# Optimization experiments

Measured on AMD Instinct MI355X. Metric: run time of the kernel, lower is better.

Reference implementation:

```python
import jax, jax.numpy as jnp
import numpy as np

HEADS = 16
KV_HEADS = 4
DIM_HEAD = 64
DIM = 1024
B, N = 2, 2048


def setup_inputs() -> dict:
    key = jax.random.key(0)
    k1, k2, k3 = jax.random.split(key, 3)
    x = jax.random.normal(k1, (B, N, DIM), dtype=jnp.float32)
    Wq = jax.random.normal(k2, (DIM, HEADS * DIM_HEAD), dtype=jnp.float32) / np.sqrt(DIM)
    Wkv = jax.random.normal(k3, (DIM, 2 * KV_HEADS * DIM_HEAD), dtype=jnp.float32) / np.sqrt(DIM)
    k_scale = jnp.ones((HEADS, 1, DIM_HEAD), dtype=jnp.float32)
    return {"x": x, "Wq": Wq, "Wkv": Wkv, "k_scale": k_scale}


def reference(x, Wq, Wkv, k_scale):
    b, n, _ = x.shape
    g = HEADS // KV_HEADS  # query heads per kv head
    scale = DIM_HEAD ** -0.5
    # fused qkv projections (no bias)
    q = (x @ Wq).reshape(b, n, HEADS, DIM_HEAD)
    kv = x @ Wkv
    k, v = jnp.split(kv, 2, axis=-1)
    k = k.reshape(b, n, KV_HEADS, DIM_HEAD).transpose(0, 2, 1, 3)  # b k n d
    v = v.reshape(b, n, KV_HEADS, DIM_HEAD).transpose(0, 2, 1, 3)  # b k n d
    # group query heads: b, kv_heads, g, n, d
    qg = q.transpose(0, 2, 1, 3).reshape(b, KV_HEADS, g, n, DIM_HEAD)
    # per-query-head k scale, applied to the group-broadcast k (qk-norm)
    ks = k_scale.reshape(KV_HEADS, g, 1, DIM_HEAD)
    kk = k[:, :, None, :, :] * ks  # b k g n d
    dots = jnp.einsum('bkgid,bkgjd->bkgij', qg, kk) * scale
    attn = jax.nn.softmax(dots, axis=-1)
    out = jnp.einsum('bkgij,bkjd->bkgid', attn, v)  # v broadcast over g
    out = out.reshape(b, HEADS, n, DIM_HEAD).transpose(0, 2, 1, 3).reshape(b, n, HEADS * DIM_HEAD)
    return out
```

## Files before the change

kernel.cpp:

```cpp
#include <hip/hip_runtime.h>
#include <stdint.h>
#include <math.h>

typedef __attribute__((ext_vector_type(8))) __bf16 bf16x8;
typedef __attribute__((ext_vector_type(4))) float f32x4;
typedef __attribute__((ext_vector_type(16))) float f32x16;

__device__ __forceinline__ uint32_t f32_to_bf16_rne(float f) {
  union { float f; uint32_t u; } v; v.f = f;
  return (v.u + 0x7FFFu + ((v.u >> 16) & 1u)) >> 16;
}

__device__ __forceinline__ uint32_t cvt_pk_bf16(float lo, float hi) {
  uint32_t r;
  asm("v_cvt_pk_bf16_f32 %0, %1, %2" : "=v"(r) : "v"(lo), "v"(hi));
  return r;
}

__device__ __forceinline__ void gld16(void* lds, const void* g) {
  __builtin_amdgcn_global_load_lds(
      (__attribute__((address_space(1))) void*)(g),
      (__attribute__((address_space(3))) void*)(lds), 16, 0, 0);
}

__device__ __forceinline__ f32x4 mfma16(bf16x8 a, bf16x8 b, f32x4 c) {
  return __builtin_amdgcn_mfma_f32_16x16x32_bf16(a, b, c, 0, 0, 0);
}
__device__ __forceinline__ f32x16 mfma32(bf16x8 a, bf16x8 b, f32x16 c) {
  return __builtin_amdgcn_mfma_f32_32x32x16_bf16(a, b, c, 0, 0, 0);
}

#define LOG2E 1.44269504088896340736f

__global__ __launch_bounds__(256) void k_convert(const float* __restrict__ x,
                                                 const float* __restrict__ wq,
                                                 const float* __restrict__ wkv,
                                                 uint16_t* __restrict__ xb,
                                                 uint16_t* __restrict__ wt) {
  __shared__ float tile[64][65];
  int blk = blockIdx.x;
  int t = threadIdx.x;
  if (blk < 2048) {
    int i = blk * 256 + t;
    const float4* xv = (const float4*)x;
    float4 a = xv[2 * i], b2 = xv[2 * i + 1];
    uint32_t w0 = f32_to_bf16_rne(a.x) | (f32_to_bf16_rne(a.y) << 16);
    uint32_t w1 = f32_to_bf16_rne(a.z) | (f32_to_bf16_rne(a.w) << 16);
    uint32_t w2 = f32_to_bf16_rne(b2.x) | (f32_to_bf16_rne(b2.y) << 16);
    uint32_t w3 = f32_to_bf16_rne(b2.z) | (f32_to_bf16_rne(b2.w) << 16);
    ((uint4*)xb)[i] = make_uint4(w0, w1, w2, w3);
  } else {
    int blk2 = blk - 2048;
    int c0 = (blk2 % 24) * 64, k0 = (blk2 / 24) * 64;
    int col = t & 63, rq = t >> 6;
#pragma unroll
    for (int rr = 0; rr < 16; rr++) {
      int r = rr * 4 + rq;
      int c = c0 + col;
      float v = (c < 1024) ? wq[(uint64_t)(k0 + r) * 1024 + c]
                           : wkv[(uint64_t)(k0 + r) * 512 + (c - 1024)];
      tile[r][col] = v;
    }
    __syncthreads();
#pragma unroll
    for (int rr = 0; rr < 16; rr++) {
      int a = rr * 4 + rq;
      wt[(uint64_t)(c0 + a) * 1024 + k0 + col] = (uint16_t)f32_to_bf16_rne(tile[col][a]);
    }
  }
}

__global__ __launch_bounds__(256, 2) void k_proj_gemm(
    const uint16_t* __restrict__ xb, const uint16_t* __restrict__ wt,
    const float* __restrict__ kscale, uint16_t* __restrict__ q_ws,
    uint16_t* __restrict__ kf_ws, uint16_t* __restrict__ vf_ws) {
  __shared__ __align__(16) uint16_t ring[3][12288];
  int t = threadIdx.x;
  int w = t >> 6, l = t & 63;
  int lq = l & 15, lg = l >> 4;
  int m0 = blockIdx.x * 128, n0 = blockIdx.y * 64;
  int wr = w >> 1, wc = w & 1;
  f32x4 acc[4][2] = {};

  auto stage = [&](int slot, int k0) {
#pragma unroll
    for (int j = 0; j < 4; j++) {
      int c = j * 256 + t;
      int r = c >> 3, s = c & 7;
      int sl = s ^ (r & 7);
      gld16((char*)&ring[slot][0] + c * 16,
            xb + (uint64_t)(m0 + r) * 1024 + k0 + sl * 8);
    }
#pragma unroll
    for (int j = 0; j < 2; j++) {
      int c = j * 256 + t;
      int r = c >> 3, s = c & 7;
      int sl = s ^ (r & 7);
      gld16((char*)&ring[slot][8192] + c * 16,
            wt + (uint64_t)(n0 + r) * 1024 + k0 + sl * 8);
    }
  };

  stage(0, 0);
  stage(1, 64);
  asm volatile("s_waitcnt vmcnt(6)" ::: "memory");
  __builtin_amdgcn_s_barrier();

  for (int it = 0; it < 16; ++it) {
    int tn = it + 2;
    int kn = (tn < 16) ? tn * 64 : (tn - 3) * 64;
    stage(tn % 3, kn);
    asm volatile("s_waitcnt vmcnt(6)" ::: "memory");
    __builtin_amdgcn_s_barrier();

    const uint16_t* As = &ring[it % 3][0];
    const uint16_t* Bs = &ring[it % 3][8192];
    bf16x8 af[2][4], bfr[2][2];
#pragma unroll
    for (int kk = 0; kk < 2; kk++) {
#pragma unroll
      for (int m = 0; m < 4; m++) {
        int r = wr * 64 + m * 16 + lq;
        int sl = (kk * 4 + lg) ^ (r & 7);
        af[kk][m] = *(const bf16x8*)(As + r * 64 + sl * 8);
      }
#pragma unroll
      for (int n = 0; n < 2; n++) {
        int r = wc * 32 + n * 16 + lq;
        int sl = (kk * 4 + lg) ^ (r & 7);
        bfr[kk][n] = *(const bf16x8*)(Bs + r * 64 + sl * 8);
      }
    }
    __builtin_amdgcn_s_setprio(1);
#pragma unroll
    for (int kk = 0; kk < 2; kk++)
#pragma unroll
      for (int m = 0; m < 4; m++)
#pragma unroll
        for (int n = 0; n < 2; n++)
          acc[m][n] = mfma16(af[kk][m], bfr[kk][n], acc[m][n]);
    __builtin_amdgcn_s_setprio(0);
  }

#pragma unroll
  for (int m = 0; m < 4; m++)
#pragma unroll
    for (int n = 0; n < 2; n++)
#pragma unroll
      for (int jj = 0; jj < 4; jj++) {
        int row = m0 + wr * 64 + m * 16 + 4 * lg + jj;
        int col = n0 + wc * 32 + n * 16 + lq;
        float val = acc[m][n][jj];
        int b = row >> 11, nn = row & 2047;
        if (col < 1024) {
          val *= kscale[col] * 0.125f * LOG2E;
          q_ws[((uint64_t)((b * 16 + (col >> 6)) * 2048 + nn)) * 64 + (col & 63)] =
              (uint16_t)f32_to_bf16_rne(val);
        } else if (col < 1280) {
          int kvh = (col - 1024) >> 6;
          int d = col & 63;
          int gsu = nn >> 5, lrr = nn & 31;
          int mm = d >> 4, hh = (d >> 3) & 1, el = d & 7;
          kf_ws[(uint64_t)(b * 4 + kvh) * 131072 +
                (uint64_t)((((gsu * 4 + mm) * 64) + hh * 32 + lrr) * 8 + el)] =
              (uint16_t)f32_to_bf16_rne(val);
        } else {
          int kvh = (col - 1280) >> 6;
          int d = col & 63;
          int gsu = nn >> 5, jj2 = (nn >> 4) & 1, hh = (nn >> 3) & 1, el = nn & 7;
          int dd = d >> 5, lrr = d & 31;
          vf_ws[(uint64_t)(b * 4 + kvh) * 131072 +
                (uint64_t)((((gsu * 4 + dd * 2 + jj2) * 64) + hh * 32 + lrr) * 8 + el)] =
              (uint16_t)f32_to_bf16_rne(val);
        }
      }
}

__global__ __launch_bounds__(512, 1) void k_attn(const uint16_t* __restrict__ q_ws,
                                                 const uint16_t* __restrict__ kf_ws,
                                                 const uint16_t* __restrict__ vf_ws,
                                                 float* __restrict__ out) {
  extern __shared__ __align__(16) char smem[];

  int t = threadIdx.x, w = t >> 6, l = t & 63;
  int lr = l & 31, hi = l >> 5;
  int qg = w & 3, half = w >> 2;
  int blk = blockIdx.x;
  int c = blk & 7, j = blk >> 3;
  int b = c >> 2, kvh = c & 3;
  int h = kvh * 4 + (j >> 3), qb = j & 7;

  const uint16_t* Qb = q_ws + (uint64_t)(b * 16 + h) * 2048 * 64;
  const uint16_t* Kb = kf_ws + (uint64_t)(b * 4 + kvh) * 131072;
  const uint16_t* Vb = vf_ws + (uint64_t)(b * 4 + kvh) * 131072;
  int qrow0 = qb * 256 + qg * 64;

  bf16x8 qfA[4], qfB[4];
#pragma unroll
  for (int m = 0; m < 4; m++) {
    qfA[m] = *(const bf16x8*)(Qb + (uint64_t)(qrow0 + lr) * 64 + m * 16 + hi * 8);
    qfB[m] = *(const bf16x8*)(Qb + (uint64_t)(qrow0 + 32 + lr) * 64 + m * 16 + hi * 8);
  }

  f32x16 oaccA[2] = {}, oaccB[2] = {};
  float lA = 0.f, lB = 0.f;

  const uint16_t* SbW = ((qg < 2) ? Kb : Vb) + (uint64_t)half * 65536 +
                        (uint64_t)((qg & 1) * 2) * 512 + l * 8;
  char* dstW = smem + half * 8192 + ((qg < 2) ? 0 : 4096) + (qg & 1) * 2048 + l * 16;

  auto stage = [&](int slot, int sul) {
    char* d = dstW + slot * 16384;
    const uint16_t* s = SbW + (uint64_t)sul * 2048;
    gld16(d, s);
    gld16(d + 1024, s + 512);
  };
  auto slotbase = [&](int slot) {
    return (const uint16_t*)(smem + slot * 16384 + half * 8192);
  };

  auto readK = [&](bf16x8* kf, const uint16_t* base) {
#pragma unroll
    for (int m = 0; m < 4; m++) kf[m] = *(const bf16x8*)(base + m * 512 + l * 8);
  };
  auto readV = [&](bf16x8* vf, const uint16_t* base) {
#pragma unroll
    for (int i = 0; i < 4; i++) vf[i] = *(const bf16x8*)(base + (4 + i) * 512 + l * 8);
  };
  auto qk = [&](const bf16x8* kf, const bf16x8* qf) {
    f32x16 T = {};
    __builtin_amdgcn_s_setprio(1);
#pragma unroll
    for (int m = 0; m < 4; m++) T = mfma32(kf[m], qf[m], T);
    __builtin_amdgcn_s_setprio(0);
    return T;
  };

  auto finish = [&](f32x16& Tc, const bf16x8* vf, f32x16* oacc, float& lsum) {
    float p[16];
#pragma unroll
    for (int e = 0; e < 16; e++) p[e] = __builtin_amdgcn_exp2f(Tc[e]);
    float sm0 = ((p[0] + p[1]) + (p[2] + p[3])) + ((p[4] + p[5]) + (p[6] + p[7]));
    float sm1 = ((p[8] + p[9]) + (p[10] + p[11])) + ((p[12] + p[13]) + (p[14] + p[15]));
    lsum += sm0 + sm1;

    bf16x8 pa[2];
#pragma unroll
    for (int jj = 0; jj < 2; jj++) {
      const float* pp = p + 8 * jj;
      uint32_t X = cvt_pk_bf16(pp[0], pp[1]);
      uint32_t Z = cvt_pk_bf16(pp[2], pp[3]);
      uint32_t Y = cvt_pk_bf16(pp[4], pp[5]);
      uint32_t W2 = cvt_pk_bf16(pp[6], pp[7]);
      asm volatile("v_permlane32_swap_b32 %0, %1" : "+v"(X), "+v"(Y));
      asm volatile("v_permlane32_swap_b32 %0, %1" : "+v"(Z), "+v"(W2));
      union { uint32_t u[4]; bf16x8 v; } pu;
      pu.u[0] = X; pu.u[1] = Z; pu.u[2] = Y; pu.u[3] = W2;
      pa[jj] = pu.v;
    }

    __builtin_amdgcn_s_setprio(1);
#pragma unroll
    for (int dd = 0; dd < 2; dd++)
#pragma unroll
      for (int jj = 0; jj < 2; jj++)
        oacc[dd] = mfma32(pa[jj], vf[dd * 2 + jj], oacc[dd]);
    __builtin_amdgcn_s_setprio(0);
  };

#pragma unroll
  for (int tt = 0; tt < 6; ++tt) stage(tt, tt);
  asm volatile("s_waitcnt vmcnt(4)" ::: "memory");
  __builtin_amdgcn_s_barrier();

  for (int iv = 0; iv < 16; ++iv) {
    int a = 2 * iv;
    int s0 = a + 6, s1 = a + 7;
    if (s0 > 31) s0 = 31;
    if (s1 > 31) s1 = 31;
    stage((a + 6) & 7, s0);
    stage((a + 7) & 7, s1);

    const uint16_t* b0 = slotbase(a & 7);
    const uint16_t* b1 = slotbase((a + 1) & 7);

    if (half == 0) {
      bf16x8 kf[4], vf[4];
      readK(kf, b0);
      readV(vf, b0);
      f32x16 Ta = qk(kf, qfA);
      f32x16 Tb = qk(kf, qfB);
      finish(Ta, vf, oaccA, lA);
      finish(Tb, vf, oaccB, lB);
      readK(kf, b1);
      readV(vf, b1);
      Ta = qk(kf, qfA);
      Tb = qk(kf, qfB);
      finish(Ta, vf, oaccA, lA);
      finish(Tb, vf, oaccB, lB);
    } else {
      bf16x8 kf0[4], kf1[4];
      readK(kf0, b0);
      readK(kf1, b1);
      f32x16 T0a = qk(kf0, qfA);
      f32x16 T0b = qk(kf0, qfB);
      f32x16 T1a = qk(kf1, qfA);
      f32x16 T1b = qk(kf1, qfB);
      bf16x8 vf[4];
      readV(vf, b0);
      finish(T0a, vf, oaccA, lA);
      finish(T0b, vf, oaccB, lB);
      readV(vf, b1);
      finish(T1a, vf, oaccA, lA);
      finish(T1b, vf, oaccB, lB);
    }

    asm volatile("s_waitcnt vmcnt(8)" ::: "memory");
    __builtin_amdgcn_s_barrier();
  }

  lA += __shfl_xor(lA, 32);
  lB += __shfl_xor(lB, 32);

  asm volatile("s_waitcnt vmcnt(0)" ::: "memory");
  __syncthreads();

  float* exch = (float*)smem;
  float* exl = (float*)(smem + 65536);
  if (half == 1) {
#pragma unroll
    for (int sub = 0; sub < 2; sub++) {
      f32x16* oacc = sub ? oaccB : oaccA;
#pragma unroll
      for (int r = 0; r < 16; r++) {
        int qr = (r & 3) + 8 * (r >> 2) + 4 * hi;
        exch[qg * 4096 + (sub * 32 + qr) * 64 + lr] = oacc[0][r];
        exch[qg * 4096 + (sub * 32 + qr) * 64 + 32 + lr] = oacc[1][r];
      }
    }
    if (hi == 0) {
      exl[qg * 64 + lr] = lA;
      exl[qg * 64 + 32 + lr] = lB;
    }
  }
  __syncthreads();
  if (half == 0) {
    lA += exl[qg * 64 + lr];
    lB += exl[qg * 64 + 32 + lr];
    float invA = 1.0f / lA, invB = 1.0f / lB;
#pragma unroll
    for (int sub = 0; sub < 2; sub++) {
      f32x16* oacc = sub ? oaccB : oaccA;
      float inv = sub ? invB : invA;
#pragma unroll
      for (int r = 0; r < 16; r++) {
        int qr = (r & 3) + 8 * (r >> 2) + 4 * hi;
        float iv = __shfl(inv, qr);
        float o0 = oacc[0][r] + exch[qg * 4096 + (sub * 32 + qr) * 64 + lr];
        float o1 = oacc[1][r] + exch[qg * 4096 + (sub * 32 + qr) * 64 + 32 + lr];
        float* orow =
            out + (uint64_t)(b * 2048 + qrow0 + sub * 32 + qr) * 1024 + h * 64 + lr;
        orow[0] = o0 * iv;
        orow[32] = o1 * iv;
      }
    }
  }
}

extern "C" void kernel_launch(void* const* d_in, const int* in_sizes, int n_in,
                              void* d_out, int out_size, void* d_ws, size_t ws_size,
                              hipStream_t stream) {
  const float* x = (const float*)d_in[0];
  const float* wq = (const float*)d_in[1];
  const float* wkv = (const float*)d_in[2];
  const float* kscale = (const float*)d_in[3];
  float* out = (float*)d_out;
  char* ws = (char*)d_ws;
  uint16_t* xb = (uint16_t*)(ws);
  uint16_t* wt = (uint16_t*)(ws + (8ull << 20));
  uint16_t* q_ws = (uint16_t*)(ws + (11ull << 20));
  uint16_t* kf_ws = (uint16_t*)(ws + (19ull << 20));
  uint16_t* vf_ws = (uint16_t*)(ws + (21ull << 20));

  static bool attr_set = false;
  if (!attr_set) {
    (void)hipFuncSetAttribute((const void*)k_attn,
                              hipFuncAttributeMaxDynamicSharedMemorySize, 131072);
    attr_set = true;
  }

  k_convert<<<2432, 256, 0, stream>>>(x, wq, wkv, xb, wt);
  k_proj_gemm<<<dim3(32, 24), 256, 0, stream>>>(xb, wt, kscale, q_ws, kf_ws, vf_ws);
  k_attn<<<256, 512, 131072, stream>>>(q_ws, kf_ws, vf_ws, out);
}
```

Before: 74.94 us.

## Give each wave a private double-buffered K/V LDS stage and drop block barriers

Each wave now loads its own full K and V tile for its key half into a private double-buffered LDS region, then consumes it without any block-wide barrier. Before, the eight waves staged tiles cooperatively into a shared 8-slot ring and synchronised every two tiles. The change removes the barrier stalls and the two per-half scheduling variants. In exchange it issues four times more global-to-LDS traffic for the same tiles and cuts prefetch depth from six tiles to one, so more load latency may be exposed.

```diff
diff --git a/kernel.cpp b/kernel.cpp
--- a/kernel.cpp
+++ b/kernel.cpp
@@ -191,8 +191,8 @@
   int h = kvh * 4 + (j >> 3), qb = j & 7;
 
   const uint16_t* Qb = q_ws + (uint64_t)(b * 16 + h) * 2048 * 64;
-  const uint16_t* Kb = kf_ws + (uint64_t)(b * 4 + kvh) * 131072;
-  const uint16_t* Vb = vf_ws + (uint64_t)(b * 4 + kvh) * 131072;
+  const uint16_t* Kh = kf_ws + (uint64_t)(b * 4 + kvh) * 131072 + (uint64_t)half * 65536;
+  const uint16_t* Vh = vf_ws + (uint64_t)(b * 4 + kvh) * 131072 + (uint64_t)half * 65536;
   int qrow0 = qb * 256 + qg * 64;
 
   bf16x8 qfA[4], qfB[4];
@@ -205,28 +205,18 @@
   f32x16 oaccA[2] = {}, oaccB[2] = {};
   float lA = 0.f, lB = 0.f;
 
-  const uint16_t* SbW = ((qg < 2) ? Kb : Vb) + (uint64_t)half * 65536 +
-                        (uint64_t)((qg & 1) * 2) * 512 + l * 8;
-  char* dstW = smem + half * 8192 + ((qg < 2) ? 0 : 4096) + (qg & 1) * 2048 + l * 16;
+  char* myLDS = smem + w * 16384;
 
   auto stage = [&](int slot, int sul) {
-    char* d = dstW + slot * 16384;
-    const uint16_t* s = SbW + (uint64_t)sul * 2048;
-    gld16(d, s);
-    gld16(d + 1024, s + 512);
+    char* d = myLDS + slot * 8192 + l * 16;
+    const uint16_t* ks = Kh + (uint64_t)sul * 2048 + l * 8;
+    const uint16_t* vs = Vh + (uint64_t)sul * 2048 + l * 8;
+#pragma unroll
+    for (int f = 0; f < 4; f++) gld16(d + f * 1024, ks + f * 512);
+#pragma unroll
+    for (int f = 0; f < 4; f++) gld16(d + 4096 + f * 1024, vs + f * 512);
   };
-  auto slotbase = [&](int slot) {
-    return (const uint16_t*)(smem + slot * 16384 + half * 8192);
-  };
-
-  auto readK = [&](bf16x8* kf, const uint16_t* base) {
-#pragma unroll
-    for (int m = 0; m < 4; m++) kf[m] = *(const bf16x8*)(base + m * 512 + l * 8);
-  };
-  auto readV = [&](bf16x8* vf, const uint16_t* base) {
-#pragma unroll
-    for (int i = 0; i < 4; i++) vf[i] = *(const bf16x8*)(base + (4 + i) * 512 + l * 8);
-  };
+
   auto qk = [&](const bf16x8* kf, const bf16x8* qf) {
     f32x16 T = {};
     __builtin_amdgcn_s_setprio(1);
@@ -268,55 +258,24 @@
     __builtin_amdgcn_s_setprio(0);
   };
 
-#pragma unroll
-  for (int tt = 0; tt < 6; ++tt) stage(tt, tt);
-  asm volatile("s_waitcnt vmcnt(4)" ::: "memory");
-  __builtin_amdgcn_s_barrier();
-
-  for (int iv = 0; iv < 16; ++iv) {
-    int a = 2 * iv;
-    int s0 = a + 6, s1 = a + 7;
-    if (s0 > 31) s0 = 31;
-    if (s1 > 31) s1 = 31;
-    stage((a + 6) & 7, s0);
-    stage((a + 7) & 7, s1);
-
-    const uint16_t* b0 = slotbase(a & 7);
-    const uint16_t* b1 = slotbase((a + 1) & 7);
-
-    if (half == 0) {
-      bf16x8 kf[4], vf[4];
-      readK(kf, b0);
-      readV(vf, b0);
-      f32x16 Ta = qk(kf, qfA);
-      f32x16 Tb = qk(kf, qfB);
-      finish(Ta, vf, oaccA, lA);
-      finish(Tb, vf, oaccB, lB);
-      readK(kf, b1);
-      readV(vf, b1);
-      Ta = qk(kf, qfA);
-      Tb = qk(kf, qfB);
-      finish(Ta, vf, oaccA, lA);
-      finish(Tb, vf, oaccB, lB);
-    } else {
-      bf16x8 kf0[4], kf1[4];
-      readK(kf0, b0);
-      readK(kf1, b1);
-      f32x16 T0a = qk(kf0, qfA);
-      f32x16 T0b = qk(kf0, qfB);
-      f32x16 T1a = qk(kf1, qfA);
-      f32x16 T1b = qk(kf1, qfB);
-      bf16x8 vf[4];
-      readV(vf, b0);
-      finish(T0a, vf, oaccA, lA);
-      finish(T0b, vf, oaccB, lB);
-      readV(vf, b1);
-      finish(T1a, vf, oaccA, lA);
-      finish(T1b, vf, oaccB, lB);
-    }
-
+  stage(0, 0);
+
+  for (int su = 0; su < 32; ++su) {
+    int sn = (su + 1 > 31) ? 31 : su + 1;
+    stage((su + 1) & 1, sn);
     asm volatile("s_waitcnt vmcnt(8)" ::: "memory");
-    __builtin_amdgcn_s_barrier();
+
+    const uint16_t* base = (const uint16_t*)(myLDS + (su & 1) * 8192);
+    bf16x8 kf[4];
+#pragma unroll
+    for (int m = 0; m < 4; m++) kf[m] = *(const bf16x8*)(base + m * 512 + l * 8);
+    f32x16 Ta = qk(kf, qfA);
+    f32x16 Tb = qk(kf, qfB);
+    bf16x8 vf[4];
+#pragma unroll
+    for (int i = 0; i < 4; i++) vf[i] = *(const bf16x8*)(base + (4 + i) * 512 + l * 8);
+    finish(Ta, vf, oaccA, lA);
+    finish(Tb, vf, oaccB, lB);
   }
 
   lA += __shfl_xor(lA, 32);
```

Result: slower. 80.82 us (+7.9%).
